# Performance work log

Hardware: AMD Instinct MI355X
Metric: run time of the kernel (lower is better)

The kernel has to match this reference:

```python
import jax, jax.numpy as jnp
import numpy as np

N, E, T = 4096, 49152, 262144
H, EMB, AIN, EB, TB = 256, 64, 92, 80, 40
NBLK = 12  # 4 alignn * 2 EGGC + 4 gcn


def _ln(x, s, b):
    mu = jnp.mean(x, -1, keepdims=True)
    v = jnp.mean((x - mu) ** 2, -1, keepdims=True)
    return (x - mu) * jax.lax.rsqrt(v + 1e-5) * s + b


def _mlp(x, W, b, s, bi):
    # Linear -> LayerNorm -> SiLU (MLPLayer)
    return jax.nn.silu(_ln(x @ W + b, s, bi))


def _rbf(x, vmin, vmax, bins):
    centers = jnp.linspace(vmin, vmax, bins)
    gamma = 1.0 / ((vmax - vmin) / (bins - 1))
    return jnp.exp(-gamma * (x[:, None] - centers) ** 2)


def _eggc(x, e, src, dst, W, b, ln_s, ln_b, n_nodes):
    # W: [5,H,H] = src_gate, dst_gate, edge_gate, src_update, dst_update
    m = (x @ W[0] + b[0])[src] + (x @ W[1] + b[1])[dst] + (e @ W[2] + b[2])
    sigma = jax.nn.sigmoid(m)
    sum_sh = jax.ops.segment_sum((x @ W[4] + b[4])[src] * sigma, dst, num_segments=n_nodes)
    sum_s = jax.ops.segment_sum(sigma, dst, num_segments=n_nodes)
    h = sum_sh / (sum_s + 1e-6)
    x_new = jax.nn.silu(_ln(x @ W[3] + b[3] + h, ln_s[0], ln_b[0]))
    e_new = jax.nn.silu(_ln(m, ln_s[1], ln_b[1]))
    return x + x_new, e + e_new  # residual=True


def setup_inputs() -> dict:
    key = jax.random.key(0)
    ks = jax.random.split(key, 16)
    s = 0.05
    return {
        "atom_features": jax.random.normal(ks[0], (N, AIN), jnp.float32),
        "r": jax.random.normal(ks[1], (E, 3), jnp.float32),
        "src": jax.random.randint(ks[2], (E,), 0, N),
        "dst": jax.random.randint(ks[3], (E,), 0, N),
        "lsrc": jax.random.randint(ks[4], (T,), 0, E),
        "ldst": jax.random.randint(ks[5], (T,), 0, E),
        "atom_W": s * jax.random.normal(ks[6], (AIN, H), jnp.float32),
        "atom_b": jnp.zeros((H,), jnp.float32),
        "atom_ln_s": jnp.ones((H,), jnp.float32),
        "atom_ln_b": jnp.zeros((H,), jnp.float32),
        "edge_W1": s * jax.random.normal(ks[7], (EB, EMB), jnp.float32),
        "edge_b1": jnp.zeros((EMB,), jnp.float32),
        "edge_ln1_s": jnp.ones((EMB,), jnp.float32),
        "edge_ln1_b": jnp.zeros((EMB,), jnp.float32),
        "edge_W2": s * jax.random.normal(ks[8], (EMB, H), jnp.float32),
        "edge_b2": jnp.zeros((H,), jnp.float32),
        "edge_ln2_s": jnp.ones((H,), jnp.float32),
        "edge_ln2_b": jnp.zeros((H,), jnp.float32),
        "ang_W1": s * jax.random.normal(ks[9], (TB, EMB), jnp.float32),
        "ang_b1": jnp.zeros((EMB,), jnp.float32),
        "ang_ln1_s": jnp.ones((EMB,), jnp.float32),
        "ang_ln1_b": jnp.zeros((EMB,), jnp.float32),
        "ang_W2": s * jax.random.normal(ks[10], (EMB, H), jnp.float32),
        "ang_b2": jnp.zeros((H,), jnp.float32),
        "ang_ln2_s": jnp.ones((H,), jnp.float32),
        "ang_ln2_b": jnp.zeros((H,), jnp.float32),
        "eggc_W": s * jax.random.normal(ks[11], (NBLK, 5, H, H), jnp.float32),
        "eggc_b": jnp.zeros((NBLK, 5, H), jnp.float32),
        "eggc_ln_s": jnp.ones((NBLK, 2, H), jnp.float32),
        "eggc_ln_b": jnp.zeros((NBLK, 2, H), jnp.float32),
        "fc_W": s * jax.random.normal(ks[12], (H, 1), jnp.float32),
        "fc_b": jnp.zeros((1,), jnp.float32),
    }


def reference(atom_features, r, src, dst, lsrc, ldst,
              atom_W, atom_b, atom_ln_s, atom_ln_b,
              edge_W1, edge_b1, edge_ln1_s, edge_ln1_b,
              edge_W2, edge_b2, edge_ln2_s, edge_ln2_b,
              ang_W1, ang_b1, ang_ln1_s, ang_ln1_b,
              ang_W2, ang_b2, ang_ln2_s, ang_ln2_b,
              eggc_W, eggc_b, eggc_ln_s, eggc_ln_b, fc_W, fc_b):
    # line-graph bond cosines: cos(-r_i, r_j) for each bond pair
    r1, r2 = -r[lsrc], r[ldst]
    cos = jnp.sum(r1 * r2, -1) / (jnp.linalg.norm(r1, axis=-1) * jnp.linalg.norm(r2, axis=-1))
    cos = jnp.clip(cos, -1.0, 1.0)
    z = _mlp(_mlp(_rbf(cos, -1.0, 1.0, TB), ang_W1, ang_b1, ang_ln1_s, ang_ln1_b),
             ang_W2, ang_b2, ang_ln2_s, ang_ln2_b)
    x = _mlp(atom_features, atom_W, atom_b, atom_ln_s, atom_ln_b)
    bondlength = jnp.linalg.norm(r, axis=1)
    y = _mlp(_mlp(_rbf(bondlength, 0.0, 8.0, EB), edge_W1, edge_b1, edge_ln1_s, edge_ln1_b),
             edge_W2, edge_b2, edge_ln2_s, edge_ln2_b)
    for i in range(4):  # alignn layers: crystal graph then line graph
        x, m = _eggc(x, y, src, dst, eggc_W[2 * i], eggc_b[2 * i], eggc_ln_s[2 * i], eggc_ln_b[2 * i], N)
        y, z = _eggc(m, z, lsrc, ldst, eggc_W[2 * i + 1], eggc_b[2 * i + 1], eggc_ln_s[2 * i + 1], eggc_ln_b[2 * i + 1], E)
    for i in range(4):  # gcn layers
        j = 8 + i
        x, y = _eggc(x, y, src, dst, eggc_W[j], eggc_b[j], eggc_ln_s[j], eggc_ln_b[j], N)
    atomwise_energy = x @ fc_W + fc_b  # [N,1]
    total_energy = jnp.mean(atomwise_energy)  # AvgPooling (eV/atom), single graph
    return total_energy, atomwise_energy
```

## Files before the change

kernel.cpp:

```cpp
#include <hip/hip_runtime.h>


typedef unsigned short bfu;
typedef __attribute__((ext_vector_type(8))) short short8;
typedef __attribute__((ext_vector_type(4))) float floatx4;

#define CHN 4096
#define CHCAP 24576
#define HH 65536

__device__ __forceinline__ float bf2f(bfu u) {
  union { unsigned u; float f; } x; x.u = ((unsigned)u) << 16; return x.f;
}
__device__ __forceinline__ bfu f2bf(float f) {
  union { float f; unsigned u; } x; x.f = f;
  unsigned r = x.u + 0x7FFFu + ((x.u >> 16) & 1u);
  return (bfu)(r >> 16);
}
__device__ __forceinline__ float fsig(float x) {
  return __builtin_amdgcn_rcpf(1.f + __expf(-x));
}
__device__ __forceinline__ float fsilu(float x) { return x * fsig(x); }

__device__ __forceinline__ void load_lds16(const bfu* g, bfu* l) {
  __builtin_amdgcn_global_load_lds(
      (const __attribute__((address_space(1))) void*)g,
      (__attribute__((address_space(3))) void*)l, 16, 0, 0);
}

struct f8 { float v[8]; };
__device__ __forceinline__ f8 ld8(const bfu* p) {
  short8 u = *(const short8*)(const void*)p;
  f8 r;
#pragma unroll
  for (int i = 0; i < 8; ++i) r.v[i] = bf2f((bfu)u[i]);
  return r;
}
__device__ __forceinline__ void st8(bfu* p, f8 x) {
  short8 u;
#pragma unroll
  for (int i = 0; i < 8; ++i) u[i] = (short)f2bf(x.v[i]);
  *(short8*)(void*)p = u;
}
__device__ __forceinline__ f8 add8(f8 a, f8 b) {
  f8 r;
#pragma unroll
  for (int i = 0; i < 8; ++i) r.v[i] = a.v[i] + b.v[i];
  return r;
}
__device__ __forceinline__ f8 sig8(f8 m) {
  f8 r;
#pragma unroll
  for (int i = 0; i < 8; ++i) r.v[i] = fsig(m.v[i]);
  return r;
}
__device__ __forceinline__ void wstats32(const f8& x, float& mean, float& rstd) {
  float s = 0.f, q = 0.f;
#pragma unroll
  for (int i = 0; i < 8; ++i) { s += x.v[i]; q += x.v[i] * x.v[i]; }
#pragma unroll
  for (int m = 1; m < 32; m <<= 1) { s += __shfl_xor(s, m); q += __shfl_xor(q, m); }
  mean = s * (1.f / 256.f);
  rstd = rsqrtf(fmaxf(q * (1.f / 256.f) - mean * mean, 0.f) + 1e-5f);
}
__device__ __forceinline__ f8 lnsilu8(f8 pre, f8 sg, f8 bb) {
  float mean, rstd; wstats32(pre, mean, rstd);
  f8 r;
#pragma unroll
  for (int i = 0; i < 8; ++i)
    r.v[i] = fsilu((pre.v[i] - mean) * rstd * sg.v[i] + bb.v[i]);
  return r;
}

__device__ __forceinline__ float block_sum256(float t, float* sm) {
#pragma unroll
  for (int o = 32; o; o >>= 1) t += __shfl_down(t, o);
  if ((threadIdx.x & 63) == 0) sm[threadIdx.x >> 6] = t;
  __syncthreads();
  float r = sm[0] + sm[1] + sm[2] + sm[3];
  __syncthreads();
  return r;
}

__global__ void probe_kernel(const unsigned* __restrict__ ones_raw, int* __restrict__ mode) {
  if (threadIdx.x == 0) *mode = (ones_raw[0] == 0x3F800000u) ? 1 : 0;
}
__global__ __launch_bounds__(256) void cvt_kernel(
    const void* __restrict__ src, bfu* __restrict__ dst, int n, const int* __restrict__ mode) {
  int i = blockIdx.x * 256 + threadIdx.x;
  if (i >= n) return;
  dst[i] = (*mode) ? f2bf(((const float*)src)[i]) : ((const bfu*)src)[i];
}
__global__ __launch_bounds__(256) void cvtf_kernel(
    const void* __restrict__ src, float* __restrict__ dst, int n, const int* __restrict__ mode) {
  int i = blockIdx.x * 256 + threadIdx.x;
  if (i >= n) return;
  dst[i] = (*mode) ? ((const float*)src)[i] : bf2f(((const bfu*)src)[i]);
}
struct CvtDesc { const void* src; bfu* dst; int n; };
struct CvtPack { CvtDesc e[20]; };
__global__ __launch_bounds__(256) void cvt_batch_kernel(CvtPack p, const int* __restrict__ mode) {
  CvtDesc d = p.e[blockIdx.y];
  int i = blockIdx.x * 256 + threadIdx.x;
  if (i >= d.n) return;
  d.dst[i] = (*mode) ? f2bf(((const float*)d.src)[i]) : ((const bfu*)d.src)[i];
}

template<int BM, int BN, int WR, int WC>
__device__ __forceinline__ void gemm_body(
    const bfu* __restrict__ A, const bfu* __restrict__ Bt,
    const bfu* __restrict__ bias, bfu* __restrict__ Cout,
    int cnt, int N, int K, int base, int m0, int n0)
{
  constexpr int WM = BM / WR, WN = BN / WC;
  constexpr int TM = WM / 16, TN = WN / 16;
  static __shared__ __align__(16) bfu As[BM * 64];
  static __shared__ __align__(16) bfu Bs[BN * 64];

  const int tid = threadIdx.x, wave = tid >> 6, lane = tid & 63;
  const int wr = wave / WC, wc = wave % WC;
  const int lrow = lane & 15, kq = (lane >> 4) * 8;

  floatx4 acc[TM][TN];
#pragma unroll
  for (int i = 0; i < TM; ++i)
#pragma unroll
    for (int j = 0; j < TN; ++j) acc[i][j] = (floatx4){0.f, 0.f, 0.f, 0.f};

  for (int k0 = 0; k0 < K; k0 += 64) {
#pragma unroll
    for (int it = 0; it < BM / 32; ++it) {
      int ch = it * 256 + tid;
      int row = ch >> 3, kc = (ch & 7) << 3;
      int r = m0 + row;
      int ar = base + (r < cnt ? r : cnt - 1);
      load_lds16(A + (size_t)ar * K + k0 + kc, As + (size_t)(it * 256 + wave * 64) * 8);
    }
#pragma unroll
    for (int it = 0; it < BN / 32; ++it) {
      int ch = it * 256 + tid;
      int row = ch >> 3, kc = (ch & 7) << 3;
      load_lds16(Bt + (size_t)(n0 + row) * K + k0 + kc, Bs + (size_t)(it * 256 + wave * 64) * 8);
    }
    __syncthreads();
#pragma unroll
    for (int s = 0; s < 2; ++s) {
      short8 Af[TM], Bf[TN];
#pragma unroll
      for (int i = 0; i < TM; ++i)
        Af[i] = *(const short8*)(const void*)(As + (wr * WM + i * 16 + lrow) * 64 + s * 32 + kq);
#pragma unroll
      for (int j = 0; j < TN; ++j)
        Bf[j] = *(const short8*)(const void*)(Bs + (wc * WN + j * 16 + lrow) * 64 + s * 32 + kq);
#pragma unroll
      for (int i = 0; i < TM; ++i)
#pragma unroll
        for (int j = 0; j < TN; ++j)
          acc[i][j] = __builtin_amdgcn_mfma_f32_16x16x32_bf16(Af[i], Bf[j], acc[i][j], 0, 0, 0);
    }
    __syncthreads();
  }

  const int rquad = lane >> 4, cin = lane & 15;
#pragma unroll
  for (int i = 0; i < TM; ++i) {
#pragma unroll
    for (int rr = 0; rr < 4; ++rr) {
      int orow = m0 + wr * WM + i * 16 + rquad * 4 + rr;
      if (orow >= cnt) continue;
#pragma unroll
      for (int j = 0; j < TN; ++j) {
        int gcol = n0 + wc * WN + j * 16 + cin;
        Cout[(size_t)orow * N + gcol] = f2bf(acc[i][j][rr] + bf2f(bias[gcol]));
      }
    }
  }
}

template<int BM, int BN, int WR, int WC>
__global__ __launch_bounds__(256) void gemm_kernel(
    const bfu* __restrict__ A, const bfu* __restrict__ Bt,
    const bfu* __restrict__ bias, bfu* __restrict__ Cout, int M, int N, int K)
{
  gemm_body<BM, BN, WR, WC>(A, Bt, bias, Cout, M, N, K, 0,
                            blockIdx.x * BM, blockIdx.y * BN);
}

__global__ __launch_bounds__(256) void line_gemm_kernel(
    const bfu* __restrict__ z, const bfu* __restrict__ yb,
    const bfu* __restrict__ W, const bfu* __restrict__ bb,
    bfu* __restrict__ mchunk, bfu* __restrict__ u3c,
    const int* __restrict__ loff, int n0, int n1)
{
  if (blockIdx.y < 2) {
    int base = loff[n0], cnt = loff[n1] - base;
    int m0 = blockIdx.x * 128;
    if (m0 >= cnt) return;
    gemm_body<128, 128, 2, 2>(z, W + 4 * HH, bb + 4 * 256, mchunk,
                              cnt, 256, 256, base, m0, blockIdx.y * 128);
  } else {
    if (blockIdx.x >= 64) return;
    gemm_body<128, 128, 2, 2>(yb + (size_t)n0 * 256, W + 3 * HH, bb + 3 * 256, u3c,
                              CHN, 256, 256, 0, (blockIdx.x & 31) * 128, (blockIdx.x >> 5) * 128);
  }
}

__global__ __launch_bounds__(256) void atom_gemm_kernel(
    const bfu* __restrict__ x, const bfu* __restrict__ y,
    const bfu* __restrict__ W, const bfu* __restrict__ bb,
    bfu* __restrict__ afused, bfu* __restrict__ mbufa)
{
  if (blockIdx.x < 384) {
    gemm_body<128, 128, 2, 2>(y, W + 4 * HH, bb + 4 * 256, mbufa,
                              49152, 256, 256, 0, blockIdx.x * 128, blockIdx.y * 128);
  } else {
    int lid = (blockIdx.x - 384) * 2 + blockIdx.y;
    gemm_body<128, 128, 2, 2>(x, W, bb, afused,
                              4096, 1024, 256, 0, (lid >> 3) * 128, (lid & 7) * 128);
  }
}

__global__ __launch_bounds__(256) void line_gates_kernel(
    const bfu* __restrict__ y, const bfu* __restrict__ z,
    const bfu* __restrict__ W, const bfu* __restrict__ bb,
    bfu* __restrict__ lfused, bfu* __restrict__ mch0, bfu* __restrict__ u3c0,
    const int* __restrict__ loff)
{
  if (blockIdx.y < 6) {
    gemm_body<128, 128, 2, 2>(y, W, bb, lfused,
                              49152, 768, 256, 0, blockIdx.x * 128, blockIdx.y * 128);
  } else if (blockIdx.y < 8) {
    int cnt = loff[CHN];
    int m0 = blockIdx.x * 128;
    if (blockIdx.x >= CHCAP / 128 || m0 >= cnt) return;
    gemm_body<128, 128, 2, 2>(z, W + 4 * HH, bb + 4 * 256, mch0,
                              cnt, 256, 256, 0, m0, (blockIdx.y - 6) * 128);
  } else {
    if (blockIdx.x >= 64) return;
    gemm_body<128, 128, 2, 2>(y, W + 3 * HH, bb + 3 * 256, u3c0,
                              CHN, 256, 256, 0, (blockIdx.x & 31) * 128, (blockIdx.x >> 5) * 128);
  }
}

__global__ __launch_bounds__(256) void cosbl_kernel(
    const float* __restrict__ r, const int* __restrict__ lsrc_p,
    const int* __restrict__ ldst_p, float* __restrict__ cosv,
    float* __restrict__ bl, int T, int E)
{
  int idx = blockIdx.x * 256 + threadIdx.x;
  if (idx < T) {
    int e1 = lsrc_p[idx], e2 = ldst_p[idx];
    float ax = -r[e1 * 3 + 0], ay = -r[e1 * 3 + 1], az = -r[e1 * 3 + 2];
    float bx =  r[e2 * 3 + 0], by =  r[e2 * 3 + 1], bz =  r[e2 * 3 + 2];
    float dot = ax * bx + ay * by + az * bz;
    float na = sqrtf(ax * ax + ay * ay + az * az);
    float nb = sqrtf(bx * bx + by * by + bz * bz);
    float c = dot / (na * nb);
    cosv[idx] = fminf(1.f, fmaxf(-1.f, c));
  } else if (idx < T + E) {
    int e = idx - T;
    float x = r[e * 3 + 0], yv = r[e * 3 + 1], zv = r[e * 3 + 2];
    bl[e] = sqrtf(x * x + yv * yv + zv * zv);
  }
}

template<int KP, int BINS, int IS_ANG>
__global__ __launch_bounds__(256) void mlp1_ln_kernel(
    const float* __restrict__ v, const bfu* __restrict__ Bt,
    const bfu* __restrict__ bias, const bfu* __restrict__ lns,
    const bfu* __restrict__ lnb, bfu* __restrict__ outp, int M)
{
  constexpr int LDT = KP + 8;
  __shared__ bfu As[128 * LDT];
  const int tid = threadIdx.x, wave = tid >> 6, lane = tid & 63;
  const int lrow = lane & 15, kq = (lane >> 4) * 8;
  const int m0 = blockIdx.x * 128;

  for (int idx = tid; idx < 128 * (KP / 8); idx += 256) {
    int row = idx / (KP / 8), kc = (idx % (KP / 8)) * 8;
    float val = v[m0 + row];
    short8 pack;
#pragma unroll
    for (int jj = 0; jj < 8; ++jj) {
      int k = kc + jj;
      float e = 0.f;
      if (k < BINS) {
        float center = IS_ANG ? (-1.f + k * (2.f / 39.f)) : (k * (8.f / 79.f));
        float d = val - center;
        e = __expf((IS_ANG ? -19.5f : -9.875f) * d * d);
      }
      pack[jj] = (short)f2bf(e);
    }
    *(short8*)(void*)(As + row * LDT + kc) = pack;
  }
  __syncthreads();

  floatx4 acc[2][4];
#pragma unroll
  for (int i = 0; i < 2; ++i)
#pragma unroll
    for (int j = 0; j < 4; ++j) acc[i][j] = (floatx4){0.f, 0.f, 0.f, 0.f};
#pragma unroll
  for (int ks = 0; ks < KP / 32; ++ks) {
    short8 Af[2], Bf[4];
#pragma unroll
    for (int j = 0; j < 4; ++j)
      Bf[j] = *(const short8*)(const void*)(Bt + (size_t)(j * 16 + lrow) * KP + ks * 32 + kq);
#pragma unroll
    for (int i = 0; i < 2; ++i)
      Af[i] = *(const short8*)(const void*)(As + (wave * 32 + i * 16 + lrow) * LDT + ks * 32 + kq);
#pragma unroll
    for (int i = 0; i < 2; ++i)
#pragma unroll
      for (int j = 0; j < 4; ++j)
        acc[i][j] = __builtin_amdgcn_mfma_f32_16x16x32_bf16(Af[i], Bf[j], acc[i][j], 0, 0, 0);
  }

  const int rquad = lane >> 4, cin = lane & 15;
  float bj[4], sj[4], lj[4];
#pragma unroll
  for (int j = 0; j < 4; ++j) {
    bj[j] = bf2f(bias[j * 16 + cin]);
    sj[j] = bf2f(lns[j * 16 + cin]);
    lj[j] = bf2f(lnb[j * 16 + cin]);
  }
#pragma unroll
  for (int i = 0; i < 2; ++i) {
#pragma unroll
    for (int rr = 0; rr < 4; ++rr) {
      int row = m0 + wave * 32 + i * 16 + rquad * 4 + rr;
      float pre[4], s = 0.f, q = 0.f;
#pragma unroll
      for (int j = 0; j < 4; ++j) {
        pre[j] = acc[i][j][rr] + bj[j];
        s += pre[j]; q += pre[j] * pre[j];
      }
#pragma unroll
      for (int mm = 1; mm < 16; mm <<= 1) { s += __shfl_xor(s, mm); q += __shfl_xor(q, mm); }
      float mean = s * (1.f / 64.f);
      float rstd = rsqrtf(fmaxf(q * (1.f / 64.f) - mean * mean, 0.f) + 1e-5f);
#pragma unroll
      for (int j = 0; j < 4; ++j) {
        float u = (pre[j] - mean) * rstd * sj[j] + lj[j];
        outp[(size_t)row * 64 + j * 16 + cin] = f2bf(fsilu(u));
      }
    }
  }
}

__global__ __launch_bounds__(256) void mlp2_ln_kernel(
    const bfu* __restrict__ A, const bfu* __restrict__ Bt,
    const bfu* __restrict__ bias, const bfu* __restrict__ lns,
    const bfu* __restrict__ lnb, bfu* __restrict__ outp, int M)
{
  __shared__ float part[64 * 8];
  const int tid = threadIdx.x, wave = tid >> 6, lane = tid & 63;
  const int lrow = lane & 15, kq = (lane >> 4) * 8;
  const int m0 = blockIdx.x * 64;

  short8 Bf[2][4];
#pragma unroll
  for (int s = 0; s < 2; ++s)
#pragma unroll
    for (int j = 0; j < 4; ++j)
      Bf[s][j] = *(const short8*)(const void*)(
          Bt + (size_t)(wave * 64 + j * 16 + lrow) * 64 + s * 32 + kq);

  floatx4 acc[4][4];
#pragma unroll
  for (int i = 0; i < 4; ++i)
#pragma unroll
    for (int j = 0; j < 4; ++j) acc[i][j] = (floatx4){0.f, 0.f, 0.f, 0.f};
#pragma unroll
  for (int s = 0; s < 2; ++s) {
    short8 Af[4];
#pragma unroll
    for (int i = 0; i < 4; ++i)
      Af[i] = *(const short8*)(const void*)(
          A + (size_t)(m0 + i * 16 + lrow) * 64 + s * 32 + kq);
#pragma unroll
    for (int i = 0; i < 4; ++i)
#pragma unroll
      for (int j = 0; j < 4; ++j)
        acc[i][j] = __builtin_amdgcn_mfma_f32_16x16x32_bf16(Af[i], Bf[s][j], acc[i][j], 0, 0, 0);
  }

  const int rquad = lane >> 4, cin = lane & 15;
  float bj[4], sj[4], lj[4];
#pragma unroll
  for (int j = 0; j < 4; ++j) {
    int col = wave * 64 + j * 16 + cin;
    bj[j] = bf2f(bias[col]); sj[j] = bf2f(lns[col]); lj[j] = bf2f(lnb[col]);
  }
#pragma unroll
  for (int i = 0; i < 4; ++i) {
#pragma unroll
    for (int rr = 0; rr < 4; ++rr) {
      float s = 0.f, q = 0.f;
#pragma unroll
      for (int j = 0; j < 4; ++j) {
        float p = acc[i][j][rr] + bj[j];
        s += p; q += p * p;
      }
#pragma unroll
      for (int mm = 1; mm < 16; mm <<= 1) { s += __shfl_xor(s, mm); q += __shfl_xor(q, mm); }
      if (cin == 0) {
        int row = i * 16 + rquad * 4 + rr;
        part[row * 8 + wave * 2] = s;
        part[row * 8 + wave * 2 + 1] = q;
      }
    }
  }
  __syncthreads();
#pragma unroll
  for (int i = 0; i < 4; ++i) {
#pragma unroll
    for (int rr = 0; rr < 4; ++rr) {
      int row = i * 16 + rquad * 4 + rr;
      float s = part[row * 8] + part[row * 8 + 2] + part[row * 8 + 4] + part[row * 8 + 6];
      float q = part[row * 8 + 1] + part[row * 8 + 3] + part[row * 8 + 5] + part[row * 8 + 7];
      float mean = s * (1.f / 256.f);
      float rstd = rsqrtf(fmaxf(q * (1.f / 256.f) - mean * mean, 0.f) + 1e-5f);
#pragma unroll
      for (int j = 0; j < 4; ++j) {
        float u = (acc[i][j][rr] + bj[j] - mean) * rstd * sj[j] + lj[j];
        outp[(size_t)(m0 + row) * 256 + wave * 64 + j * 16 + cin] = f2bf(fsilu(u));
      }
    }
  }
}

__global__ __launch_bounds__(256) void count_kernel(
    const int* __restrict__ d, int* __restrict__ cnt, int ne) {
  int i = blockIdx.x * 256 + threadIdx.x;
  if (i < ne) atomicAdd(&cnt[d[i]], 1);
}
__global__ __launch_bounds__(256) void scan_kernel(
    const int* __restrict__ cnt, int* __restrict__ off, int n) {
  __shared__ int ssum[256];
  __shared__ int sbase[257];
  int t = threadIdx.x;
  int strip = (n + 255) / 256;
  int lo = t * strip, hi = lo + strip; if (hi > n) hi = n; if (lo > n) lo = n;
  int s = 0;
  for (int i = lo; i < hi; ++i) s += cnt[i];
  ssum[t] = s;
  __syncthreads();
  if (t == 0) {
    int run = 0;
    for (int i = 0; i < 256; ++i) { sbase[i] = run; run += ssum[i]; }
    sbase[256] = run;
  }
  __syncthreads();
  int run = sbase[t];
  for (int i = lo; i < hi; ++i) { off[i] = run; run += cnt[i]; }
  if (t == 0) off[n] = sbase[256];
}
__global__ __launch_bounds__(256) void copy_kernel(
    const int* __restrict__ a, int* __restrict__ b, int n) {
  int i = blockIdx.x * 256 + threadIdx.x;
  if (i < n) b[i] = a[i];
}
__global__ __launch_bounds__(256) void fill_kernel(
    const int* __restrict__ d, int* __restrict__ cur, int* __restrict__ ids, int ne) {
  int i = blockIdx.x * 256 + threadIdx.x;
  if (i < ne) ids[atomicAdd(&cur[d[i]], 1)] = i;
}
__global__ __launch_bounds__(256) void fill2_kernel(
    const int* __restrict__ ldst, const int* __restrict__ lsrc, int* __restrict__ cur,
    int* __restrict__ lsrc_p, int* __restrict__ ldst_p, int ne) {
  int i = blockIdx.x * 256 + threadIdx.x;
  if (i >= ne) return;
  int d = ldst[i];
  int pos = atomicAdd(&cur[d], 1);
  lsrc_p[pos] = lsrc[i];
  ldst_p[pos] = d;
}

__global__ __launch_bounds__(256) void transpose_pad_kernel(
    const void* __restrict__ W, bfu* __restrict__ Wt, int K, int N, int Kp,
    const int* __restrict__ mode)
{
  int idx = blockIdx.x * 256 + threadIdx.x;
  if (idx >= N * Kp) return;
  int n = idx / Kp, k = idx - n * Kp;
  bfu v = 0;
  if (k < K) {
    size_t si = (size_t)k * N + n;
    v = (*mode) ? f2bf(((const float*)W)[si]) : ((const bfu*)W)[si];
  }
  Wt[idx] = v;
}
__device__ __forceinline__ int slot2mat(int slot) {
  const int m[5] = {0, 4, 1, 3, 2};
  return m[slot];
}
__global__ __launch_bounds__(256) void transpose_eggc_kernel(
    const void* __restrict__ W, bfu* __restrict__ Wt, const int* __restrict__ mode)
{
  int bs = blockIdx.y;
  int blk = bs / 5, slot = bs - blk * 5;
  int mat = slot2mat(slot);
  int idx = blockIdx.x * 256 + threadIdx.x;
  int n = idx >> 8, k = idx & 255;
  size_t si = ((size_t)(blk * 5 + mat) * 256 + k) * 256 + n;
  bfu v = (*mode) ? f2bf(((const float*)W)[si]) : ((const bfu*)W)[si];
  Wt[((size_t)bs * 256 + n) * 256 + k] = v;
}
__global__ __launch_bounds__(256) void bias_perm_kernel(
    const void* __restrict__ B, bfu* __restrict__ Bp, const int* __restrict__ mode)
{
  int i = blockIdx.x * 256 + threadIdx.x;
  int bs = i >> 8, c = i & 255;
  int blk = bs / 5, slot = bs - blk * 5;
  int mat = slot2mat(slot);
  size_t si = (size_t)(blk * 5 + mat) * 256 + c;
  Bp[i] = (*mode) ? f2bf(((const float*)B)[si]) : ((const bfu*)B)[si];
}

__global__ __launch_bounds__(256) void atom_fused_kernel(
    const bfu* __restrict__ mbuf, const bfu* __restrict__ af,
    const int* __restrict__ src, const int* __restrict__ dst,
    bfu* __restrict__ X, bfu* __restrict__ Y,
    const int* __restrict__ aoff, const int* __restrict__ aids,
    int eblk,
    const bfu* __restrict__ lns, const bfu* __restrict__ lnb,
    const bfu* __restrict__ les, const bfu* __restrict__ leb)
{
  int wave = threadIdx.x >> 6, lane = threadIdx.x & 63;
  int half = lane >> 5, c8 = (lane & 31) * 8;
  if ((int)blockIdx.x < eblk) {
    int e = blockIdx.x * 8 + wave * 2 + half;
    f8 m = add8(add8(ld8(mbuf + (size_t)e * 256 + c8),
                     ld8(af + (size_t)src[e] * 1024 + c8)),
                ld8(af + (size_t)dst[e] * 1024 + 512 + c8));
    f8 sil = lnsilu8(m, ld8(les + c8), ld8(leb + c8));
    bfu* op = Y + (size_t)e * 256 + c8;
    st8(op, add8(sil, ld8(op)));
  } else {
    int n = (blockIdx.x - eblk) * 4 + wave;
    int p0 = aoff[n], p1 = aoff[n + 1];
    f8 g1 = ld8(af + (size_t)n * 1024 + 512 + c8);
    f8 num = {}, den = {};
    for (int p = p0 + half; p < p1; p += 2) {
      int id = aids[p], sx = src[id];
      f8 m = add8(add8(ld8(mbuf + (size_t)id * 256 + c8),
                       ld8(af + (size_t)sx * 1024 + c8)), g1);
      f8 sg = sig8(m);
      f8 u4 = ld8(af + (size_t)sx * 1024 + 256 + c8);
#pragma unroll
      for (int i = 0; i < 8; ++i) {
        num.v[i] += sg.v[i] * u4.v[i];
        den.v[i] += sg.v[i];
      }
    }
#pragma unroll
    for (int i = 0; i < 8; ++i) {
      num.v[i] += __shfl_xor(num.v[i], 32);
      den.v[i] += __shfl_xor(den.v[i], 32);
    }
    f8 u3 = ld8(af + (size_t)n * 1024 + 768 + c8);
    f8 pre;
#pragma unroll
    for (int i = 0; i < 8; ++i)
      pre.v[i] = u3.v[i] + num.v[i] / (den.v[i] + 1e-6f);
    f8 sil = lnsilu8(pre, ld8(lns + c8), ld8(lnb + c8));
    if (half == 0) {
      bfu* op = X + (size_t)n * 256 + c8;
      st8(op, add8(sil, ld8(op)));
    }
  }
}

__global__ __launch_bounds__(256) void line_fused_kernel(
    const bfu* __restrict__ mchunk, const bfu* __restrict__ lf,
    const bfu* __restrict__ u3c,
    const int* __restrict__ loff, const int* __restrict__ lsrc_p,
    const int* __restrict__ ldst_p,
    bfu* __restrict__ Z, bfu* __restrict__ Y,
    int n0, int eblk,
    const bfu* __restrict__ lns, const bfu* __restrict__ lnb,
    const bfu* __restrict__ les, const bfu* __restrict__ leb)
{
  int wave = threadIdx.x >> 6, lane = threadIdx.x & 63;
  int half = lane >> 5, c8 = (lane & 31) * 8;
  int base = loff[n0];
  if ((int)blockIdx.x < eblk) {
    int rloc = blockIdx.x * 8 + wave * 2 + half;
    int cnt = loff[n0 + CHN] - base;
    if (rloc >= cnt) return;
    int p = base + rloc;
    f8 m = add8(add8(ld8(mchunk + (size_t)rloc * 256 + c8),
                     ld8(lf + (size_t)lsrc_p[p] * 768 + c8)),
                ld8(lf + (size_t)ldst_p[p] * 768 + 512 + c8));
    f8 sil = lnsilu8(m, ld8(les + c8), ld8(leb + c8));
    bfu* op = Z + (size_t)p * 256 + c8;
    st8(op, add8(sil, ld8(op)));
  } else {
    int n = n0 + (blockIdx.x - eblk) * 4 + wave;
    int p0 = loff[n], p1 = loff[n + 1];
    f8 g1 = ld8(lf + (size_t)n * 768 + 512 + c8);
    f8 num = {}, den = {};
    for (int p = p0 + half; p < p1; p += 2) {
      int sx = lsrc_p[p];
      f8 m = add8(add8(ld8(mchunk + (size_t)(p - base) * 256 + c8),
                       ld8(lf + (size_t)sx * 768 + c8)), g1);
      f8 sg = sig8(m);
      f8 u4 = ld8(lf + (size_t)sx * 768 + 256 + c8);
#pragma unroll
      for (int i = 0; i < 8; ++i) {
        num.v[i] += sg.v[i] * u4.v[i];
        den.v[i] += sg.v[i];
      }
    }
#pragma unroll
    for (int i = 0; i < 8; ++i) {
      num.v[i] += __shfl_xor(num.v[i], 32);
      den.v[i] += __shfl_xor(den.v[i], 32);
    }
    f8 u3 = ld8(u3c + (size_t)(n - n0) * 256 + c8);
    f8 pre;
#pragma unroll
    for (int i = 0; i < 8; ++i)
      pre.v[i] = u3.v[i] + num.v[i] / (den.v[i] + 1e-6f);
    f8 sil = lnsilu8(pre, ld8(lns + c8), ld8(lnb + c8));
    if (half == 0) {
      bfu* op = Y + (size_t)n * 256 + c8;
      st8(op, add8(sil, ld8(op)));
    }
  }
}

__global__ __launch_bounds__(256) void atom_init_kernel(
    const bfu* __restrict__ af, const bfu* __restrict__ W, const bfu* __restrict__ bias,
    const bfu* __restrict__ lns, const bfu* __restrict__ lnb, bfu* __restrict__ X)
{
  __shared__ float sm[4];
  int row = blockIdx.x, c = threadIdx.x;
  float acc = bf2f(bias[c]);
  for (int k = 0; k < 92; ++k)
    acc += bf2f(af[row * 92 + k]) * bf2f(W[k * 256 + c]);
  float mean = block_sum256(acc, sm) * (1.f / 256.f);
  float d = acc - mean;
  float var = block_sum256(d * d, sm) * (1.f / 256.f);
  float u = d * rsqrtf(var + 1e-5f) * bf2f(lns[c]) + bf2f(lnb[c]);
  X[(size_t)row * 256 + c] = f2bf(fsilu(u));
}

__global__ __launch_bounds__(256) void final_kernel(
    const bfu* __restrict__ X, const bfu* __restrict__ fcW, const bfu* __restrict__ fcb,
    void* __restrict__ out, float* __restrict__ acc, const int* __restrict__ mode)
{
  int row = blockIdx.x * 4 + (threadIdx.x >> 6);
  int lane = threadIdx.x & 63;
  float s = 0.f;
#pragma unroll
  for (int k = 0; k < 4; ++k)
    s += bf2f(X[(size_t)row * 256 + lane + k * 64]) * bf2f(fcW[lane + k * 64]);
#pragma unroll
  for (int o = 32; o; o >>= 1) s += __shfl_down(s, o);
  if (lane == 0) {
    float v = s + bf2f(fcb[0]);
    if (*mode) ((float*)out)[1 + row] = v;
    else       ((bfu*)out)[1 + row] = f2bf(v);
    atomicAdd(acc, v);
  }
}
__global__ void mean_kernel(const float* __restrict__ acc, void* __restrict__ out,
                            const int* __restrict__ mode) {
  if (threadIdx.x == 0) {
    float v = acc[0] * (1.f / 4096.f);
    if (*mode) ((float*)out)[0] = v;
    else       ((bfu*)out)[0] = f2bf(v);
  }
}
__global__ void dbg_kernel(void* __restrict__ out, float v) {
  if (threadIdx.x == 0) { ((bfu*)out)[0] = f2bf(v); }
}

extern "C" void kernel_launch(void* const* d_in, const int* in_sizes, int n_in,
                              void* d_out, int out_size, void* d_ws, size_t ws_size,
                              hipStream_t stream) {
  const int N = 4096, E = 49152, T = 262144, H = 256;

  const int* src  = (const int*)d_in[2];
  const int* dst  = (const int*)d_in[3];
  const int* lsrc = (const int*)d_in[4];
  const int* ldst = (const int*)d_in[5];

  char* bp = (char*)d_ws;
  size_t off = 0;
  auto carve = [&](size_t bytes) -> char* {
    char* q = bp + off;
    off = (off + bytes + 255) & ~(size_t)255;
    return q;
  };
  bfu* x       = (bfu*)carve((size_t)N * H * 2);
  bfu* y       = (bfu*)carve((size_t)E * H * 2);
  bfu* z       = (bfu*)carve((size_t)T * H * 2);
  bfu* reg     = (bfu*)carve((size_t)E * 768 * 2);
  bfu* u3c     = (bfu*)carve((size_t)CHN * H * 2);
  bfu* mchunk  = (bfu*)carve((size_t)CHCAP * H * 2);
  bfu* WtE     = (bfu*)carve((size_t)60 * H * H * 2);
  bfu* ebp     = (bfu*)carve((size_t)12 * 5 * H * 2);
  bfu* Wt_a1   = (bfu*)carve(64 * 64 * 2);
  bfu* Wt_a2   = (bfu*)carve(256 * 64 * 2);
  bfu* Wt_e1   = (bfu*)carve(64 * 128 * 2);
  bfu* Wt_e2   = (bfu*)carve(256 * 64 * 2);
  int* aoff    = (int*)carve((size_t)(N + 1) * 4);
  int* aids    = (int*)carve((size_t)E * 4);
  int* loff    = (int*)carve((size_t)(E + 1) * 4);
  int* lsrc_p  = (int*)carve((size_t)T * 4);
  int* ldst_p  = (int*)carve((size_t)T * 4);
  int* cursors = (int*)carve((size_t)E * 4);
  float* macc  = (float*)carve(256);
  int* mode    = (int*)carve(256);
  bfu* par_c   = (bfu*)carve(8192 * 2);
  bfu* els_c   = (bfu*)carve((size_t)12 * 2 * H * 2);
  bfu* elb_c   = (bfu*)carve((size_t)12 * 2 * H * 2);

  if (off > ws_size) {
    hipMemsetAsync(d_out, 0, (size_t)out_size * 2, stream);
    dbg_kernel<<<1, 64, 0, stream>>>(d_out, (float)(ws_size >> 20));
    return;
  }

  char* tail = (char*)reg + (size_t)52 * 1024 * 1024;
  bfu* af_c  = (bfu*)tail;                 tail += ((size_t)N * 92 * 2 + 255) & ~255ull;
  float* r_f = (float*)tail;               tail += ((size_t)E * 3 * 4 + 255) & ~255ull;
  float* cosv = (float*)tail;              tail += ((size_t)T * 4 + 255) & ~255ull;
  float* blv = (float*)tail;               tail += ((size_t)E * 4 + 255) & ~255ull;
  bfu* atW_c = (bfu*)tail;

  bfu* atom_b_c   = par_c + 0;
  bfu* atom_lns_c = par_c + 256;
  bfu* atom_lnb_c = par_c + 512;
  bfu* e_b1_c     = par_c + 768;
  bfu* e_l1s_c    = par_c + 832;
  bfu* e_l1b_c    = par_c + 896;
  bfu* e_b2_c     = par_c + 1024;
  bfu* e_l2s_c    = par_c + 1280;
  bfu* e_l2b_c    = par_c + 1536;
  bfu* a_b1_c     = par_c + 1792;
  bfu* a_l1s_c    = par_c + 1856;
  bfu* a_l1b_c    = par_c + 1920;
  bfu* a_b2_c     = par_c + 2048;
  bfu* a_l2s_c    = par_c + 2304;
  bfu* a_l2b_c    = par_c + 2560;
  bfu* fcW_c      = par_c + 2816;
  bfu* fcb_c      = par_c + 3072;

  bfu* lfused = reg;
  bfu* afused = reg;
  bfu* mbufa  = reg + (size_t)N * 1024;
  bfu* emb_t  = reg;
  bfu* emb_e  = reg + (size_t)T * 64;

  probe_kernel<<<1, 64, 0, stream>>>((const unsigned*)d_in[8], mode);
  CvtPack pk;
  int ii = 0;
  auto add = [&](int idx, bfu* dstp, int n) { pk.e[ii++] = {d_in[idx], dstp, n}; };
  add(7, atom_b_c, 256);  add(8, atom_lns_c, 256); add(9, atom_lnb_c, 256);
  add(11, e_b1_c, 64);    add(12, e_l1s_c, 64);    add(13, e_l1b_c, 64);
  add(15, e_b2_c, 256);   add(16, e_l2s_c, 256);   add(17, e_l2b_c, 256);
  add(19, a_b1_c, 64);    add(20, a_l1s_c, 64);    add(21, a_l1b_c, 64);
  add(23, a_b2_c, 256);   add(24, a_l2s_c, 256);   add(25, a_l2b_c, 256);
  add(30, fcW_c, 256);    add(31, fcb_c, 1);
  add(28, els_c, 12 * 2 * 256);
  add(29, elb_c, 12 * 2 * 256);
  add(6, atW_c, 92 * 256);
  cvt_batch_kernel<<<dim3(92, 20), 256, 0, stream>>>(pk, mode);
  cvt_kernel<<<(N * 92 + 255) / 256, 256, 0, stream>>>(d_in[0], af_c, N * 92, mode);
  cvtf_kernel<<<(E * 3 + 255) / 256, 256, 0, stream>>>(d_in[1], r_f, E * 3, mode);

  hipMemsetAsync(cursors, 0, (size_t)N * 4, stream);
  count_kernel<<<E / 256, 256, 0, stream>>>(dst, cursors, E);
  scan_kernel<<<1, 256, 0, stream>>>(cursors, aoff, N);
  copy_kernel<<<(N + 255) / 256, 256, 0, stream>>>(aoff, cursors, N);
  fill_kernel<<<E / 256, 256, 0, stream>>>(dst, cursors, aids, E);

  hipMemsetAsync(cursors, 0, (size_t)E * 4, stream);
  count_kernel<<<T / 256, 256, 0, stream>>>(ldst, cursors, T);
  scan_kernel<<<1, 256, 0, stream>>>(cursors, loff, E);
  copy_kernel<<<(E + 255) / 256, 256, 0, stream>>>(loff, cursors, E);
  fill2_kernel<<<T / 256, 256, 0, stream>>>(ldst, lsrc, cursors, lsrc_p, ldst_p, T);

  transpose_eggc_kernel<<<dim3(256, 60), 256, 0, stream>>>(d_in[26], WtE, mode);
  bias_perm_kernel<<<60, 256, 0, stream>>>(d_in[27], ebp, mode);
  transpose_pad_kernel<<<16, 256, 0, stream>>>(d_in[18], Wt_a1, 40, 64, 64, mode);
  transpose_pad_kernel<<<64, 256, 0, stream>>>(d_in[22], Wt_a2, 64, 256, 64, mode);
  transpose_pad_kernel<<<32, 256, 0, stream>>>(d_in[10], Wt_e1, 80, 64, 128, mode);
  transpose_pad_kernel<<<64, 256, 0, stream>>>(d_in[14], Wt_e2, 64, 256, 64, mode);

  cosbl_kernel<<<(T + E + 255) / 256, 256, 0, stream>>>(r_f, lsrc_p, ldst_p, cosv, blv, T, E);
  mlp1_ln_kernel<64, 40, 1><<<T / 128, 256, 0, stream>>>(
      cosv, Wt_a1, a_b1_c, a_l1s_c, a_l1b_c, emb_t, T);
  mlp2_ln_kernel<<<T / 64, 256, 0, stream>>>(emb_t, Wt_a2, a_b2_c, a_l2s_c, a_l2b_c, z, T);
  mlp1_ln_kernel<128, 80, 0><<<E / 128, 256, 0, stream>>>(
      blv, Wt_e1, e_b1_c, e_l1s_c, e_l1b_c, emb_e, E);
  mlp2_ln_kernel<<<E / 64, 256, 0, stream>>>(emb_e, Wt_e2, e_b2_c, e_l2s_c, e_l2b_c, y, E);

  atom_init_kernel<<<N, 256, 0, stream>>>(af_c, atW_c, atom_b_c, atom_lns_c, atom_lnb_c, x);

  auto atom_eggc = [&](int blk, int do_edge) {
    const bfu* W  = WtE + (size_t)blk * 5 * HH;
    const bfu* bb = ebp + (size_t)blk * 5 * H;
    const bfu* ls = els_c + (size_t)blk * 2 * H;
    const bfu* lb = elb_c + (size_t)blk * 2 * H;
    atom_gemm_kernel<<<dim3(512, 2), 256, 0, stream>>>(x, y, W, bb, afused, mbufa);
    int eblk = do_edge ? E / 8 : 0;
    atom_fused_kernel<<<eblk + N / 4, 256, 0, stream>>>(
        mbufa, afused, src, dst, x, y, aoff, aids, eblk, ls, lb, ls + H, lb + H);
  };

  auto line_eggc = [&](int blk, int do_edge) {
    const bfu* W  = WtE + (size_t)blk * 5 * HH;
    const bfu* bb = ebp + (size_t)blk * 5 * H;
    const bfu* ls = els_c + (size_t)blk * 2 * H;
    const bfu* lb = elb_c + (size_t)blk * 2 * H;
    line_gates_kernel<<<dim3(384, 9), 256, 0, stream>>>(
        y, z, W, bb, lfused, mchunk, u3c, loff);
    for (int c = 0; c < E / CHN; ++c) {
      int n0 = c * CHN;
      int eblk = do_edge ? CHCAP / 8 : 0;
      line_fused_kernel<<<eblk + CHN / 4, 256, 0, stream>>>(
          mchunk, lfused, u3c, loff, lsrc_p, ldst_p, z, y, n0, eblk,
          ls, lb, ls + H, lb + H);
      if (c + 1 < E / CHN)
        line_gemm_kernel<<<dim3(CHCAP / 128, 3), 256, 0, stream>>>(
            z, y, W, bb, mchunk, u3c, loff, n0 + CHN, n0 + 2 * CHN);
    }
  };

  for (int i = 0; i < 4; ++i) {
    atom_eggc(2 * i, 1);
    line_eggc(2 * i + 1, i < 3);
  }
  for (int i = 0; i < 4; ++i)
    atom_eggc(8 + i, i < 3);

  hipMemsetAsync(macc, 0, 4, stream);
  final_kernel<<<N / 4, 256, 0, stream>>>(x, fcW_c, fcb_c, d_out, macc, mode);
  mean_kernel<<<1, 64, 0, stream>>>(macc, d_out, mode);
}
```

Baseline: 2.619 ms.

## Fuse edge update into dst-sorted aggregation loop reusing gate pre-activation

The edge-update branch, which ran as separate blocks and recomputed m by gathering the src and dst node features, is folded into the per-node aggregation loop. There m is already computed for each incoming edge, so the edge LayerNorm-SiLU residual update is applied in place, removing the extra gathers and the dst index reads. The risk is that edge writes are now scattered in dst-sorted order (via aids in the atom kernel), the node loop carries more work per iteration, and there are fewer, less balanced blocks.

```diff
diff --git a/kernel.cpp b/kernel.cpp
--- a/kernel.cpp
+++ b/kernel.cpp
@@ -520,55 +520,52 @@
 
 __global__ __launch_bounds__(256) void atom_fused_kernel(
     const bfu* __restrict__ mbuf, const bfu* __restrict__ af,
-    const int* __restrict__ src, const int* __restrict__ dst,
+    const int* __restrict__ src,
     bfu* __restrict__ X, bfu* __restrict__ Y,
     const int* __restrict__ aoff, const int* __restrict__ aids,
-    int eblk,
+    int do_edge,
     const bfu* __restrict__ lns, const bfu* __restrict__ lnb,
     const bfu* __restrict__ les, const bfu* __restrict__ leb)
 {
   int wave = threadIdx.x >> 6, lane = threadIdx.x & 63;
   int half = lane >> 5, c8 = (lane & 31) * 8;
-  if ((int)blockIdx.x < eblk) {
-    int e = blockIdx.x * 8 + wave * 2 + half;
-    f8 m = add8(add8(ld8(mbuf + (size_t)e * 256 + c8),
-                     ld8(af + (size_t)src[e] * 1024 + c8)),
-                ld8(af + (size_t)dst[e] * 1024 + 512 + c8));
-    f8 sil = lnsilu8(m, ld8(les + c8), ld8(leb + c8));
-    bfu* op = Y + (size_t)e * 256 + c8;
+  int n = blockIdx.x * 4 + wave;
+  int p0 = aoff[n], p1 = aoff[n + 1];
+  f8 g1 = ld8(af + (size_t)n * 1024 + 512 + c8);
+  f8 esg = {}, ebb = {};
+  if (do_edge) { esg = ld8(les + c8); ebb = ld8(leb + c8); }
+  f8 num = {}, den = {};
+  for (int p = p0 + half; p < p1; p += 2) {
+    int id = aids[p], sx = src[id];
+    f8 m = add8(add8(ld8(mbuf + (size_t)id * 256 + c8),
+                     ld8(af + (size_t)sx * 1024 + c8)), g1);
+    f8 sg = sig8(m);
+    f8 u4 = ld8(af + (size_t)sx * 1024 + 256 + c8);
+#pragma unroll
+    for (int i = 0; i < 8; ++i) {
+      num.v[i] += sg.v[i] * u4.v[i];
+      den.v[i] += sg.v[i];
+    }
+    if (do_edge) {
+      f8 sil = lnsilu8(m, esg, ebb);
+      bfu* op = Y + (size_t)id * 256 + c8;
+      st8(op, add8(sil, ld8(op)));
+    }
+  }
+#pragma unroll
+  for (int i = 0; i < 8; ++i) {
+    num.v[i] += __shfl_xor(num.v[i], 32);
+    den.v[i] += __shfl_xor(den.v[i], 32);
+  }
+  f8 u3 = ld8(af + (size_t)n * 1024 + 768 + c8);
+  f8 pre;
+#pragma unroll
+  for (int i = 0; i < 8; ++i)
+    pre.v[i] = u3.v[i] + num.v[i] / (den.v[i] + 1e-6f);
+  f8 sil = lnsilu8(pre, ld8(lns + c8), ld8(lnb + c8));
+  if (half == 0) {
+    bfu* op = X + (size_t)n * 256 + c8;
     st8(op, add8(sil, ld8(op)));
-  } else {
-    int n = (blockIdx.x - eblk) * 4 + wave;
-    int p0 = aoff[n], p1 = aoff[n + 1];
-    f8 g1 = ld8(af + (size_t)n * 1024 + 512 + c8);
-    f8 num = {}, den = {};
-    for (int p = p0 + half; p < p1; p += 2) {
-      int id = aids[p], sx = src[id];
-      f8 m = add8(add8(ld8(mbuf + (size_t)id * 256 + c8),
-                       ld8(af + (size_t)sx * 1024 + c8)), g1);
-      f8 sg = sig8(m);
-      f8 u4 = ld8(af + (size_t)sx * 1024 + 256 + c8);
-#pragma unroll
-      for (int i = 0; i < 8; ++i) {
-        num.v[i] += sg.v[i] * u4.v[i];
-        den.v[i] += sg.v[i];
-      }
-    }
-#pragma unroll
-    for (int i = 0; i < 8; ++i) {
-      num.v[i] += __shfl_xor(num.v[i], 32);
-      den.v[i] += __shfl_xor(den.v[i], 32);
-    }
-    f8 u3 = ld8(af + (size_t)n * 1024 + 768 + c8);
-    f8 pre;
-#pragma unroll
-    for (int i = 0; i < 8; ++i)
-      pre.v[i] = u3.v[i] + num.v[i] / (den.v[i] + 1e-6f);
-    f8 sil = lnsilu8(pre, ld8(lns + c8), ld8(lnb + c8));
-    if (half == 0) {
-      bfu* op = X + (size_t)n * 256 + c8;
-      st8(op, add8(sil, ld8(op)));
-    }
   }
 }
 
@@ -576,58 +573,50 @@
     const bfu* __restrict__ mchunk, const bfu* __restrict__ lf,
     const bfu* __restrict__ u3c,
     const int* __restrict__ loff, const int* __restrict__ lsrc_p,
-    const int* __restrict__ ldst_p,
     bfu* __restrict__ Z, bfu* __restrict__ Y,
-    int n0, int eblk,
+    int n0, int do_edge,
     const bfu* __restrict__ lns, const bfu* __restrict__ lnb,
     const bfu* __restrict__ les, const bfu* __restrict__ leb)
 {
   int wave = threadIdx.x >> 6, lane = threadIdx.x & 63;
   int half = lane >> 5, c8 = (lane & 31) * 8;
-  int base = loff[n0];
-  if ((int)blockIdx.x < eblk) {
-    int rloc = blockIdx.x * 8 + wave * 2 + half;
-    int cnt = loff[n0 + CHN] - base;
-    if (rloc >= cnt) return;
-    int p = base + rloc;
-    f8 m = add8(add8(ld8(mchunk + (size_t)rloc * 256 + c8),
-                     ld8(lf + (size_t)lsrc_p[p] * 768 + c8)),
-                ld8(lf + (size_t)ldst_p[p] * 768 + 512 + c8));
-    f8 sil = lnsilu8(m, ld8(les + c8), ld8(leb + c8));
-    bfu* op = Z + (size_t)p * 256 + c8;
+  int n = n0 + blockIdx.x * 4 + wave;
+  int p0 = loff[n], p1 = loff[n + 1], base = loff[n0];
+  f8 g1 = ld8(lf + (size_t)n * 768 + 512 + c8);
+  f8 esg = {}, ebb = {};
+  if (do_edge) { esg = ld8(les + c8); ebb = ld8(leb + c8); }
+  f8 num = {}, den = {};
+  for (int p = p0 + half; p < p1; p += 2) {
+    int sx = lsrc_p[p];
+    f8 m = add8(add8(ld8(mchunk + (size_t)(p - base) * 256 + c8),
+                     ld8(lf + (size_t)sx * 768 + c8)), g1);
+    f8 sg = sig8(m);
+    f8 u4 = ld8(lf + (size_t)sx * 768 + 256 + c8);
+#pragma unroll
+    for (int i = 0; i < 8; ++i) {
+      num.v[i] += sg.v[i] * u4.v[i];
+      den.v[i] += sg.v[i];
+    }
+    if (do_edge) {
+      f8 sil = lnsilu8(m, esg, ebb);
+      bfu* op = Z + (size_t)p * 256 + c8;
+      st8(op, add8(sil, ld8(op)));
+    }
+  }
+#pragma unroll
+  for (int i = 0; i < 8; ++i) {
+    num.v[i] += __shfl_xor(num.v[i], 32);
+    den.v[i] += __shfl_xor(den.v[i], 32);
+  }
+  f8 u3 = ld8(u3c + (size_t)(n - n0) * 256 + c8);
+  f8 pre;
+#pragma unroll
+  for (int i = 0; i < 8; ++i)
+    pre.v[i] = u3.v[i] + num.v[i] / (den.v[i] + 1e-6f);
+  f8 sil = lnsilu8(pre, ld8(lns + c8), ld8(lnb + c8));
+  if (half == 0) {
+    bfu* op = Y + (size_t)n * 256 + c8;
     st8(op, add8(sil, ld8(op)));
-  } else {
-    int n = n0 + (blockIdx.x - eblk) * 4 + wave;
-    int p0 = loff[n], p1 = loff[n + 1];
-    f8 g1 = ld8(lf + (size_t)n * 768 + 512 + c8);
-    f8 num = {}, den = {};
-    for (int p = p0 + half; p < p1; p += 2) {
-      int sx = lsrc_p[p];
-      f8 m = add8(add8(ld8(mchunk + (size_t)(p - base) * 256 + c8),
-                       ld8(lf + (size_t)sx * 768 + c8)), g1);
-      f8 sg = sig8(m);
-      f8 u4 = ld8(lf + (size_t)sx * 768 + 256 + c8);
-#pragma unroll
-      for (int i = 0; i < 8; ++i) {
-        num.v[i] += sg.v[i] * u4.v[i];
-        den.v[i] += sg.v[i];
-      }
-    }
-#pragma unroll
-    for (int i = 0; i < 8; ++i) {
-      num.v[i] += __shfl_xor(num.v[i], 32);
-      den.v[i] += __shfl_xor(den.v[i], 32);
-    }
-    f8 u3 = ld8(u3c + (size_t)(n - n0) * 256 + c8);
-    f8 pre;
-#pragma unroll
-    for (int i = 0; i < 8; ++i)
-      pre.v[i] = u3.v[i] + num.v[i] / (den.v[i] + 1e-6f);
-    f8 sil = lnsilu8(pre, ld8(lns + c8), ld8(lnb + c8));
-    if (half == 0) {
-      bfu* op = Y + (size_t)n * 256 + c8;
-      st8(op, add8(sil, ld8(op)));
-    }
   }
 }
 
@@ -808,9 +797,8 @@
     const bfu* ls = els_c + (size_t)blk * 2 * H;
     const bfu* lb = elb_c + (size_t)blk * 2 * H;
     atom_gemm_kernel<<<dim3(512, 2), 256, 0, stream>>>(x, y, W, bb, afused, mbufa);
-    int eblk = do_edge ? E / 8 : 0;
-    atom_fused_kernel<<<eblk + N / 4, 256, 0, stream>>>(
-        mbufa, afused, src, dst, x, y, aoff, aids, eblk, ls, lb, ls + H, lb + H);
+    atom_fused_kernel<<<N / 4, 256, 0, stream>>>(
+        mbufa, afused, src, x, y, aoff, aids, do_edge, ls, lb, ls + H, lb + H);
   };
 
   auto line_eggc = [&](int blk, int do_edge) {
@@ -822,9 +810,8 @@
         y, z, W, bb, lfused, mchunk, u3c, loff);
     for (int c = 0; c < E / CHN; ++c) {
       int n0 = c * CHN;
-      int eblk = do_edge ? CHCAP / 8 : 0;
-      line_fused_kernel<<<eblk + CHN / 4, 256, 0, stream>>>(
-          mchunk, lfused, u3c, loff, lsrc_p, ldst_p, z, y, n0, eblk,
+      line_fused_kernel<<<CHN / 4, 256, 0, stream>>>(
+          mchunk, lfused, u3c, loff, lsrc_p, z, y, n0, do_edge,
           ls, lb, ls + H, lb + H);
       if (c + 1 < E / CHN)
         line_gemm_kernel<<<dim3(CHCAP / 128, 3), 256, 0, stream>>>(
```

Measured after the change: 2.564 ms. 2.1% less time.
